# Performance work log

Measured on AMD Instinct MI355X. Metric: run time of the kernel, lower is better.

The kernel has to match this reference:

```python
import jax, jax.numpy as jnp
import numpy as np

ALPHA = 0.2
NEG = -9e15


def _gru(x, Wih, Whh, bih, bhh):
    # x: [B, T, F]; PyTorch nn.GRU cell equations, scan over time.
    H = Whh.shape[1]
    xg = jnp.einsum('btf,gf->btg', x, Wih) + bih  # [B,T,3H]

    def step(h, gi):
        gh = h @ Whh.T + bhh
        ir, iz, inn = jnp.split(gi, 3, axis=-1)
        hr, hz, hn = jnp.split(gh, 3, axis=-1)
        r = jax.nn.sigmoid(ir + hr)
        z = jax.nn.sigmoid(iz + hz)
        n = jnp.tanh(inn + r * hn)
        h = (1.0 - z) * n + z * h
        return h, h

    h0 = jnp.zeros((x.shape[0], H), x.dtype)
    _, ys = jax.lax.scan(step, h0, jnp.swapaxes(xg, 0, 1))
    return jnp.swapaxes(ys, 0, 1)  # [B,T,H]


def _gru_attn(x, Wih, Whh, bih, bhh, aw, ab):
    out = _gru(x, Wih, Whh, bih, bhh)              # [B,T,H]
    w = jax.nn.softmax(out @ aw + ab, axis=1)       # [B,T,1]
    return jnp.sum(out * w, axis=1)                 # [B,H]


def _gat(h, mask, W, a):
    # GraphAttentionLayer with concat=True: elu(softmax(mask(leakyrelu(Wh1+Wh2^T))) @ Wh)
    Wh = h @ W                                      # [N,O]
    O = W.shape[1]
    e = jax.nn.leaky_relu((Wh @ a[:O]) + (Wh @ a[O:]).T, ALPHA)  # [N,N]
    att = jax.nn.softmax(jnp.where(mask, e, NEG), axis=1)
    return jax.nn.elu(att @ Wh)


def setup_inputs() -> dict:
    key = jax.random.key(0)
    ks = iter(jax.random.split(key, 40))
    B, S, Wk, D, F = 1, 2048, 32, 5, 16
    H, E, NS = 128, 128, 16

    def rn(shape, scale=0.1):
        return jax.random.normal(next(ks), shape, jnp.float32) * scale

    inp = {
        'stock_features': jax.random.normal(next(ks), (B, S, Wk, D, F), jnp.float32),
        'stock_to_sector': jax.random.randint(next(ks), (S,), 0, NS, jnp.int32),
        'inter_adj': jax.random.randint(next(ks), (NS, NS), 0, 2, jnp.int32),
        'gru1_Wih': rn((3 * H, F)), 'gru1_Whh': rn((3 * H, H)),
        'gru1_bih': rn((3 * H,)), 'gru1_bhh': rn((3 * H,)),
        'attn1_w': rn((H, 1)), 'attn1_b': rn((1,)),
        'gat_intra_W': rn((H, E)), 'gat_intra_a': rn((2 * E, 1)),
        'grug_Wih': rn((3 * E, E)), 'grug_Whh': rn((3 * E, E)),
        'grug_bih': rn((3 * E,)), 'grug_bhh': rn((3 * E,)),
        'attng_w': rn((E, 1)), 'attng_b': rn((1,)),
        'grua_Wih': rn((3 * E, H)), 'grua_Whh': rn((3 * E, E)),
        'grua_bih': rn((3 * E,)), 'grua_bhh': rn((3 * E,)),
        'attna_w': rn((E, 1)), 'attna_b': rn((1,)),
        'gat_inter_W': rn((E, E)), 'gat_inter_a': rn((2 * E, 1)),
        'fusion_w': rn((3 * E, E)), 'fusion_b': rn((E,)),
        'ret_w': rn((E, 1)), 'ret_b': rn((1,)),
        'mov_w': rn((E, 1)), 'mov_b': rn((1,)),
    }
    return inp


def reference(stock_features, stock_to_sector, inter_adj,
              gru1_Wih, gru1_Whh, gru1_bih, gru1_bhh, attn1_w, attn1_b,
              gat_intra_W, gat_intra_a,
              grug_Wih, grug_Whh, grug_bih, grug_bhh, attng_w, attng_b,
              grua_Wih, grua_Whh, grua_bih, grua_bhh, attna_w, attna_b,
              gat_inter_W, gat_inter_a,
              fusion_w, fusion_b, ret_w, ret_b, mov_w, mov_b):
    B, S, Wk, D, F = stock_features.shape
    H = gru1_Whh.shape[1]
    E = gat_intra_W.shape[1]
    NS = inter_adj.shape[0]

    # Short-term: GRU-attention over days, vectorized over (batch, stock, week).
    x = stock_features.reshape(B * S * Wk, D, F)
    short = _gru_attn(x, gru1_Wih, gru1_Whh, gru1_bih, gru1_bhh, attn1_w, attn1_b)
    short = short.reshape(B, S, Wk, H)

    # Intra-sector GAT on last-week embeddings; per-sector softmax == block mask.
    same_sector = stock_to_sector[:, None] == stock_to_sector[None, :]  # [S,S]
    last = short[:, :, -1, :]                                            # [B,S,H]
    intra = jax.vmap(lambda h: _gat(h, same_sector, gat_intra_W, gat_intra_a))(last)  # [B,S,E]

    # Long-term GRU-attentions.
    lg = _gru_attn(intra.reshape(B * S, 1, E), grug_Wih, grug_Whh, grug_bih, grug_bhh,
                   attng_w, attng_b).reshape(B, S, E)
    la = _gru_attn(short.reshape(B * S, Wk, H), grua_Wih, grua_Whh, grua_bih, grua_bhh,
                   attna_w, attna_b).reshape(B, S, E)

    # Sector embeddings = mean of stock long-term embeddings per sector.
    def sector_mean(g):
        sums = jax.ops.segment_sum(g, stock_to_sector, num_segments=NS)
        cnt = jax.ops.segment_sum(jnp.ones((g.shape[0], 1), g.dtype),
                                  stock_to_sector, num_segments=NS)
        return sums / jnp.maximum(cnt, 1.0)

    sec = jax.vmap(sector_mean)(lg)                                      # [B,NS,E]
    imask = inter_adj > 0
    sec_out = jax.vmap(lambda h: _gat(h, imask, gat_inter_W, gat_inter_a))(sec)
    sec_ps = sec_out[:, stock_to_sector, :]                               # [B,S,E]

    fused = jnp.concatenate([lg, la, sec_ps], axis=-1) @ fusion_w + fusion_b
    returns = (fused @ ret_w + ret_b)[..., 0]
    moves = jax.nn.sigmoid(fused @ mov_w + mov_b)[..., 0]
    return jnp.stack([returns, moves])  # [2,B,S]
```

## Files before the change

kernel.cpp:

```cpp
#include <hip/hip_runtime.h>
#include <math.h>

#define LRELU_A 0.2f
#define NEGBIG (-9.0e15f)

typedef _Float16 f16;
typedef _Float16 f16x8 __attribute__((ext_vector_type(8)));
typedef _Float16 f16x4 __attribute__((ext_vector_type(4)));
typedef _Float16 f16x2 __attribute__((ext_vector_type(2)));
typedef float floatx4 __attribute__((ext_vector_type(4)));

__device__ __forceinline__ float rcpf(float x){ return __builtin_amdgcn_rcpf(x); }
__device__ __forceinline__ float sigm(float x){ return rcpf(1.0f+__expf(-x)); }
__device__ __forceinline__ float gru_fuse(float xr, float xz, float xn_pre, float ghn, float h){
    float Er = __expf(-xr);
    float r  = rcpf(1.0f + Er);
    float En = __expf(2.0f*(xn_pre + r*ghn));
    float Ez = __expf(-xz);
    float Dn = En + 1.0f;
    float num = fmaf(h, Dn, (En - 1.0f)*Ez);
    float den = Dn * (1.0f + Ez);
    return num * rcpf(den);
}
__device__ __forceinline__ f16x8 load_cvt8(const float* __restrict__ p){
    float4 a = *(const float4*)p; float4 b = *(const float4*)(p+4);
    f16x8 r; r[0]=(f16)a.x; r[1]=(f16)a.y; r[2]=(f16)a.z; r[3]=(f16)a.w;
    r[4]=(f16)b.x; r[5]=(f16)b.y; r[6]=(f16)b.z; r[7]=(f16)b.w;
    return r;
}
#define MFMA16(A,B,C) __builtin_amdgcn_mfma_f32_16x16x32_f16((A),(B),(C),0,0,0)

__global__ __launch_bounds__(256) void prep1_kernel(
    const float* __restrict__ g1Wih, const float* __restrict__ g1Whh,
    f16* __restrict__ Wcat1)
{
    const int b = blockIdx.x, tid = threadIdx.x;
    for (int idx = b*256+tid; idx < 512*160; idx += 160*256){
        int r = idx/160, k = idx - r*160;
        float v = 0.0f;
        if (r < 256){ if (k < 32){ if (k < 16) v = g1Wih[r*16+k]; } else v = g1Whh[r*128 + (k-32)]; }
        else if (r < 384){ if (k < 16) v = g1Wih[r*16+k]; }
        else { if (k >= 32) v = g1Whh[(r-128)*128 + (k-32)]; }
        Wcat1[idx] = (f16)v;
    }
}

__global__ __launch_bounds__(512,2) void gru_short(
    const float* __restrict__ x, const f16* __restrict__ Wcat,
    const float* __restrict__ bih, const float* __restrict__ bhh,
    const float* __restrict__ aw, const float* __restrict__ ab,
    f16* __restrict__ out,
    const float* __restrict__ gaWih, const float* __restrict__ gaWhh,
    const float* __restrict__ giW,   const float* __restrict__ fw,
    const float* __restrict__ geW,   const float* __restrict__ ggWih,
    const int* __restrict__ sec,
    f16* __restrict__ WcatA, f16* __restrict__ WTp, f16* __restrict__ fwp,
    f16* __restrict__ gep,   f16* __restrict__ ggp,
    int* __restrict__ memflat, int* __restrict__ pos,
    int* __restrict__ cnt, int* __restrict__ base)
{
    __shared__ __align__(16) f16 xs[5][32][40];
    __shared__ __align__(16) f16 hs[2][32][136];
    __shared__ float scpart[2][8][32];
    __shared__ int cs[16], wsc[16];
    const int tid = threadIdx.x, w = tid>>6, lane = tid&63;
    const int c = lane&15, quad = lane>>4;

    if (blockIdx.x >= 256){
        const int b2 = blockIdx.x - 256;
        if (b2 < 256){
            int idx = b2*512 + tid;
            int r = idx >> 8, k = idx & 255;
            float v = 0.0f;
            if (r < 256){ v = (k < 128) ? gaWih[r*128+k] : gaWhh[r*128 + (k-128)]; }
            else if (r < 384){ if (k < 128) v = gaWih[r*128+k]; }
            else { if (k >= 128) v = gaWhh[(r-128)*128 + (k-128)]; }
            WcatA[idx] = (f16)v;
        } else if (b2 < 288){
            int idx = (b2-256)*512 + tid;
            int e=idx&7, ln=(idx>>3)&63, fr=idx>>9;
            int kb=fr&3, jb=fr>>2;
            int k = kb*32 + (ln>>4)*8 + e, col = jb*16 + (ln&15);
            WTp[idx] = (f16)giW[k*128 + col];
        } else if (b2 < 384){
            int idx = (b2-288)*512 + tid;
            int e=idx&7, ln=(idx>>3)&63, fr=idx>>9;
            int kb=fr%12, jb=fr/12;
            int k = kb*32 + (ln>>4)*8 + e, col = jb*16 + (ln&15);
            fwp[idx] = (f16)fw[k*128 + col];
        } else if (b2 < 416){
            int idx = (b2-384)*512 + tid;
            int e=idx&7, ln=(idx>>3)&63, fr=idx>>9;
            int kb=fr&3, jb=fr>>2;
            int k = kb*32 + (ln>>4)*8 + e, col = jb*16 + (ln&15);
            gep[idx] = (f16)geW[k*128 + col];
        } else if (b2 < 512){
            int idx = (b2-416)*512 + tid;
            int e=idx&7, ln=(idx>>3)&63, fr=idx>>9;
            int kb=fr&3, jb=(fr>>2)&7, G=fr>>5;
            int row = G*128 + jb*16 + (ln&15), k = kb*32 + (ln>>4)*8 + e;
            ggp[idx] = (f16)ggWih[row*128 + k];
        } else {
            if (tid < 16) cs[tid] = 0;
            __syncthreads();
            for (int s = tid; s < 2048; s += 512) atomicAdd(&cs[sec[s]], 1);
            __syncthreads();
            if (tid == 0){
                int acc = 0;
                for (int g=0; g<16; g++){ cnt[g]=cs[g]; base[g]=acc; wsc[g]=acc; acc+=cs[g]; }
            }
            __syncthreads();
            for (int s = tid; s < 2048; s += 512){
                int g = sec[s];
                int p2 = atomicAdd(&wsc[g], 1);
                memflat[p2] = s;
                pos[s] = p2;
            }
        }
        return;
    }
    { f16x4 z4 = {0,0,0,0};
      f16x4* zx = (f16x4*)&xs[0][0][0];
      for (int i=tid; i<1600; i+=512) zx[i] = z4; }

    const int jrow = w*16 + c;
    f16x8 Ar[5], Az[5], Agi, Agh[4];
#pragma unroll
    for (int kb=0;kb<5;kb++){
        Ar[kb] = *(const f16x8*)&Wcat[(size_t)(jrow)*160 + kb*32 + quad*8];
        Az[kb] = *(const f16x8*)&Wcat[(size_t)(128+jrow)*160 + kb*32 + quad*8];
    }
    Agi = *(const f16x8*)&Wcat[(size_t)(256+jrow)*160 + quad*8];
#pragma unroll
    for (int i=0;i<4;i++)
        Agh[i] = *(const f16x8*)&Wcat[(size_t)(384+jrow)*160 + 32 + i*32 + quad*8];

    float brz_r[4], brz_z[4], b_in[4], b_hn[4], awr[4];
#pragma unroll
    for (int r=0;r<4;r++){
        int j = w*16 + quad*4 + r;
        brz_r[r] = bih[j] + bhh[j];
        brz_z[r] = bih[128+j] + bhh[128+j];
        b_in[r] = bih[256+j]; b_hn[r] = bhh[256+j];
        awr[r] = aw[j];
    }
    const float abv = ab[0];

    const int s0i = tid/20,        q0 = tid - 20*s0i;
    const int i1  = tid + 512;
    const int s1i = i1/20,         q1 = i1 - 20*s1i;
    const bool pf1 = (tid < 128);
    float4 xpf0, xpf1;
    {
        const size_t base0 = (size_t)(blockIdx.x*8)*32;
        xpf0 = *(const float4*)&x[(base0 + s0i)*80 + q0*4];
        if (pf1) xpf1 = *(const float4*)&x[(base0 + s1i)*80 + q1*4];
    }

#pragma unroll 1
    for (int tile=0; tile<8; ++tile){
        const int s0 = (blockIdx.x*8 + tile)*32;
        {
            int t = (q0*4)>>4, f = (q0*4)&15;
            f16x4 h4; h4[0]=(f16)xpf0.x; h4[1]=(f16)xpf0.y; h4[2]=(f16)xpf0.z; h4[3]=(f16)xpf0.w;
            *(f16x4*)&xs[t][s0i][f] = h4;
            if (pf1){
                int t1 = (q1*4)>>4, f1 = (q1*4)&15;
                f16x4 g4; g4[0]=(f16)xpf1.x; g4[1]=(f16)xpf1.y; g4[2]=(f16)xpf1.z; g4[3]=(f16)xpf1.w;
                *(f16x4*)&xs[t1][s1i][f1] = g4;
            }
        }
        if (tile < 7){
            const size_t basen = (size_t)(s0 + 32);
            xpf0 = *(const float4*)&x[(basen + s0i)*80 + q0*4];
            if (pf1) xpf1 = *(const float4*)&x[(basen + s1i)*80 + q1*4];
        }
        float hreg[2][4], aacc[2][4], l_[2] = {0.0f, 0.0f};
#pragma unroll
        for (int st=0; st<2; st++)
#pragma unroll
            for (int r=0;r<4;r++){ aacc[st][r]=0.0f; }
        __syncthreads();

        {
            float sp[2];
#pragma unroll
            for (int st=0; st<2; st++){
                f16x8 Bx = *(const f16x8*)&xs[0][st*16+c][quad*8];
                floatx4 ar = {0,0,0,0}, az = {0,0,0,0}, agi = {0,0,0,0};
                ar = MFMA16(Ar[0], Bx, ar);
                az = MFMA16(Az[0], Bx, az);
                agi = MFMA16(Agi, Bx, agi);
                f16x4 h4;
                sp[st] = 0.0f;
#pragma unroll
                for (int r=0;r<4;r++){
                    float hn = gru_fuse(ar[r] + brz_r[r], az[r] + brz_z[r],
                                        agi[r] + b_in[r], b_hn[r], 0.0f);
                    hreg[st][r] = hn; h4[r] = (f16)hn;
                    sp[st] += hn * awr[r];
                }
                *(f16x4*)&hs[0][st*16 + c][w*16 + quad*4] = h4;
            }
#pragma unroll
            for (int st=0; st<2; st++){
                sp[st] += __shfl_xor(sp[st], 16);
                sp[st] += __shfl_xor(sp[st], 32);
            }
            if (lane < 16){ scpart[0][w][lane] = sp[0]; scpart[0][w][16+lane] = sp[1]; }
            __syncthreads();
        }

#pragma unroll 1
        for (int t=1; t<5; ++t){
            const int rp = (t&1)^1, wp = t&1;
            f16x8 Bx[2], Bh[2][4];
#pragma unroll
            for (int st=0; st<2; st++){
                Bx[st] = *(const f16x8*)&xs[t][st*16+c][quad*8];
#pragma unroll
                for (int i=0;i<4;i++)
                    Bh[st][i] = *(const f16x8*)&hs[rp][st*16+c][i*32+quad*8];
            }
            {
#pragma unroll
                for (int st=0; st<2; st++){
                    float sc = abv;
#pragma unroll
                    for (int ww=0; ww<8; ww++) sc += scpart[rp][ww][st*16+c];
                    float e = __expf(sc);
                    l_[st] += e;
#pragma unroll
                    for (int r=0;r<4;r++) aacc[st][r] += e*hreg[st][r];
                }
            }
            float sp[2];
#pragma unroll
            for (int st=0; st<2; st++){
                floatx4 ar = {0,0,0,0}, az = {0,0,0,0}, agi = {0,0,0,0}, agh = {0,0,0,0};
                ar = MFMA16(Ar[0], Bx[st], ar);
                az = MFMA16(Az[0], Bx[st], az);
                agi = MFMA16(Agi, Bx[st], agi);
#pragma unroll
                for (int i=0;i<4;i++){
                    ar = MFMA16(Ar[1+i], Bh[st][i], ar);
                    az = MFMA16(Az[1+i], Bh[st][i], az);
                    agh = MFMA16(Agh[i], Bh[st][i], agh);
                }
                f16x4 h4;
                sp[st] = 0.0f;
#pragma unroll
                for (int r=0;r<4;r++){
                    float hn = gru_fuse(ar[r] + brz_r[r], az[r] + brz_z[r],
                                        agi[r] + b_in[r], agh[r] + b_hn[r], hreg[st][r]);
                    hreg[st][r] = hn; h4[r] = (f16)hn;
                    sp[st] += hn * awr[r];
                }
                *(f16x4*)&hs[wp][st*16 + c][w*16 + quad*4] = h4;
            }
#pragma unroll
            for (int st=0; st<2; st++){
                sp[st] += __shfl_xor(sp[st], 16);
                sp[st] += __shfl_xor(sp[st], 32);
            }
            if (lane < 16){ scpart[wp][w][lane] = sp[0]; scpart[wp][w][16+lane] = sp[1]; }
            __syncthreads();
        }
#pragma unroll
        for (int st=0; st<2; st++){
            float sc = abv;
#pragma unroll
            for (int ww=0; ww<8; ww++) sc += scpart[0][ww][st*16+c];
            float e = __expf(sc);
            l_[st] += e;
            float inv = rcpf(l_[st]);
            f16x4 h4;
#pragma unroll
            for (int r=0;r<4;r++) h4[r] = (f16)((aacc[st][r] + e*hreg[st][r])*inv);
            *(f16x4*)&out[(size_t)(s0 + st*16 + c)*128 + w*16 + quad*4] = h4;
        }
    }
}

__global__ __launch_bounds__(512,2) void gru_la_gatprep(
    const f16* __restrict__ xseq, const f16* __restrict__ Wcat,
    const float* __restrict__ bih, const float* __restrict__ bhh,
    const float* __restrict__ aw, const float* __restrict__ ab,
    f16* __restrict__ out,
    const f16* __restrict__ WTp, const float* __restrict__ gia,
    const int* __restrict__ memflat,
    f16* __restrict__ Whs, float* __restrict__ ers, float* __restrict__ el)
{
    __shared__ __align__(16) f16 xs[2][16][136];
    __shared__ __align__(16) f16 hs[2][16][136];
    __shared__ float scpart[2][8][16];
    __shared__ __align__(16) float tbuf[32][132];
    __shared__ int rows[32];
    const int tid = threadIdx.x, w = tid>>6, lane = tid&63;
    const int c = lane&15, quad = lane>>4;

    if (blockIdx.x >= 256){
        const int p0 = (blockIdx.x-256)*32;
        if (tid < 32) rows[tid] = memflat[p0 + tid];
        __syncthreads();
        f16x8 A[2][4];
#pragma unroll
        for (int mt=0;mt<2;mt++)
#pragma unroll
            for (int kb=0;kb<4;kb++)
                A[mt][kb] = *(const f16x8*)&xseq[((size_t)rows[mt*16+c]*32 + 31)*128 + kb*32 + quad*8];
        {
            f16x8 B[4];
#pragma unroll
            for (int kb=0;kb<4;kb++)
                B[kb] = *(const f16x8*)&WTp[(((size_t)(w*4+kb))*64 + lane)*8];
            floatx4 acc[2] = {{0,0,0,0},{0,0,0,0}};
#pragma unroll
            for (int kb=0;kb<4;kb++){
                acc[0] = MFMA16(A[0][kb], B[kb], acc[0]);
                acc[1] = MFMA16(A[1][kb], B[kb], acc[1]);
            }
#pragma unroll
            for (int mt=0;mt<2;mt++)
#pragma unroll
                for (int r=0;r<4;r++)
                    tbuf[mt*16 + quad*4 + r][w*16 + c] = acc[mt][r];
        }
        __syncthreads();
        for (int i=tid; i<1024; i+=512){
            int s = i>>5, p = i&31;
            float4 v = *(const float4*)&tbuf[s][p*4];
            f16x4 h4; h4[0]=(f16)v.x; h4[1]=(f16)v.y; h4[2]=(f16)v.z; h4[3]=(f16)v.w;
            *(f16x4*)&Whs[(size_t)(p0+s)*128 + p*4] = h4;
        }
        for (int k=0; k<4; k++){
            int row = w*4 + k;
            float w0 = tbuf[row][lane], w1 = tbuf[row][64+lane];
            float v1 = w0*gia[lane]     + w1*gia[64+lane];
            float v2 = w0*gia[128+lane] + w1*gia[192+lane];
#pragma unroll
            for (int off=32; off; off>>=1){ v1 += __shfl_down(v1,off); v2 += __shfl_down(v2,off); }
            if (lane==0){ el[rows[row]] = v1; ers[p0+row] = v2; }
        }
        return;
    }
    const int s0 = blockIdx.x*8;
    if (tid < 128){
        int s = tid>>4, p = tid&15;
        *(f16x8*)&xs[0][s][p*8] = *(const f16x8*)&xseq[((size_t)(s0+s)*32 + 0)*128 + p*8];
    }
    const int jrow = w*16 + c;
    f16x8 Ar[8], Az[8], Agi[4], Agh[4];
#pragma unroll
    for (int kb=0;kb<8;kb++){
        Ar[kb] = *(const f16x8*)&Wcat[(size_t)(jrow)*256 + kb*32 + quad*8];
        Az[kb] = *(const f16x8*)&Wcat[(size_t)(128+jrow)*256 + kb*32 + quad*8];
    }
#pragma unroll
    for (int i=0;i<4;i++){
        Agi[i] = *(const f16x8*)&Wcat[(size_t)(256+jrow)*256 + i*32 + quad*8];
        Agh[i] = *(const f16x8*)&Wcat[(size_t)(384+jrow)*256 + 128 + i*32 + quad*8];
    }
    float brz_r[4], brz_z[4], b_in[4], b_hn[4], awr[4];
#pragma unroll
    for (int r=0;r<4;r++){
        int j = w*16 + quad*4 + r;
        brz_r[r] = bih[j] + bhh[j];
        brz_z[r] = bih[128+j] + bhh[128+j];
        b_in[r] = bih[256+j]; b_hn[r] = bhh[256+j];
        awr[r] = aw[j];
    }
    const float abv = ab[0];
    float hreg[4] = {0,0,0,0}, aacc[4] = {0,0,0,0}, l_ = 0.0f;
    __syncthreads();

    {
        f16x8 Bx[4];
#pragma unroll
        for (int i=0;i<4;i++) Bx[i] = *(const f16x8*)&xs[0][c][i*32+quad*8];
        f16x8 xstage;
        if (tid < 128){
            int s = tid>>4, p = tid&15;
            xstage = *(const f16x8*)&xseq[((size_t)(s0+s)*32 + 1)*128 + p*8];
        }
        floatx4 ar = {0,0,0,0}, az = {0,0,0,0}, agi = {0,0,0,0};
#pragma unroll
        for (int i=0;i<4;i++){
            ar  = MFMA16(Ar[i],  Bx[i], ar);
            az  = MFMA16(Az[i],  Bx[i], az);
            agi = MFMA16(Agi[i], Bx[i], agi);
        }
        f16x4 h4;
        float sp = 0.0f;
#pragma unroll
        for (int r=0;r<4;r++){
            float hn = gru_fuse(ar[r] + brz_r[r], az[r] + brz_z[r],
                                agi[r] + b_in[r], b_hn[r], 0.0f);
            hreg[r] = hn; h4[r] = (f16)hn;
            sp += hn * awr[r];
        }
        *(f16x4*)&hs[0][c][w*16 + quad*4] = h4;
        if (tid < 128){
            int s = tid>>4, p = tid&15;
            *(f16x8*)&xs[1][s][p*8] = xstage;
        }
        sp += __shfl_xor(sp, 16);
        sp += __shfl_xor(sp, 32);
        if (lane < 16) scpart[0][w][lane] = sp;
        __syncthreads();
    }

#pragma unroll 1
    for (int t=1; t<32; ++t){
        const int rp = (t&1)^1, wp = t&1, xp = t&1;
        f16x8 Bx[4], Bh[4];
#pragma unroll
        for (int i=0;i<4;i++){
            Bx[i] = *(const f16x8*)&xs[xp][c][i*32+quad*8];
            Bh[i] = *(const f16x8*)&hs[rp][c][i*32+quad*8];
        }
        f16x8 xstage;
        const bool do_stage = (t < 31) && (tid < 128);
        if (do_stage){
            int s = tid>>4, p = tid&15;
            xstage = *(const f16x8*)&xseq[((size_t)(s0+s)*32 + t+1)*128 + p*8];
        }
        {
            float sc = abv;
#pragma unroll
            for (int ww=0; ww<8; ww++) sc += scpart[rp][ww][c];
            float e = __expf(sc);
            l_ += e;
#pragma unroll
            for (int r=0;r<4;r++) aacc[r] += e*hreg[r];
        }
        floatx4 ar = {0,0,0,0}, az = {0,0,0,0}, agi = {0,0,0,0}, agh = {0,0,0,0};
#pragma unroll
        for (int i=0;i<4;i++){
            ar = MFMA16(Ar[i], Bx[i], ar);
            az = MFMA16(Az[i], Bx[i], az);
            agi = MFMA16(Agi[i], Bx[i], agi);
        }
#pragma unroll
        for (int i=0;i<4;i++){
            ar = MFMA16(Ar[4+i], Bh[i], ar);
            az = MFMA16(Az[4+i], Bh[i], az);
            agh = MFMA16(Agh[i], Bh[i], agh);
        }
        f16x4 h4;
        float sp = 0.0f;
#pragma unroll
        for (int r=0;r<4;r++){
            float hn = gru_fuse(ar[r] + brz_r[r], az[r] + brz_z[r],
                                agi[r] + b_in[r], agh[r] + b_hn[r], hreg[r]);
            hreg[r] = hn; h4[r] = (f16)hn;
            sp += hn * awr[r];
        }
        *(f16x4*)&hs[wp][c][w*16 + quad*4] = h4;
        if (do_stage){
            int s = tid>>4, p = tid&15;
            *(f16x8*)&xs[xp^1][s][p*8] = xstage;
        }
        sp += __shfl_xor(sp, 16);
        sp += __shfl_xor(sp, 32);
        if (lane < 16) scpart[wp][w][lane] = sp;
        __syncthreads();
    }
    {
        float sc = abv;
#pragma unroll
        for (int ww=0; ww<8; ww++) sc += scpart[1][ww][c];
        float e = __expf(sc);
        l_ += e;
        float inv = rcpf(l_);
        f16x4 h4;
#pragma unroll
        for (int r=0;r<4;r++) h4[r] = (f16)((aacc[r] + e*hreg[r])*inv);
        if (c < 8)
            *(f16x4*)&out[(size_t)(s0 + c)*128 + w*16 + quad*4] = h4;
    }
}

__global__ __launch_bounds__(256) void gat_intra_mem_kernel(
    const f16* __restrict__ Whs, const float* __restrict__ ers,
    const float* __restrict__ el, const int* __restrict__ sec,
    const int* __restrict__ cnt, const int* __restrict__ base,
    f16* __restrict__ outp, int S)
{
    int wave = threadIdx.x>>6, lane = threadIdx.x&63;
    int i = blockIdx.x*4 + wave;
    if (i>=S) return;
    int g = sec[i];
    int n = cnt[g], b = base[g];
    float eli = el[i];
    float m = -INFINITY;
    for (int jj=lane; jj<n; jj+=64){
        float v = eli + ers[b+jj]; v = v>0.f? v : LRELU_A*v;
        m = fmaxf(m, v);
    }
#pragma unroll
    for (int off=32; off; off>>=1) m = fmaxf(m, __shfl_xor(m, off));
    float l = 0.f, c0=0.f, c1=0.f;
#pragma unroll 8
    for (int jj=0; jj<n; jj++){
        float v = eli + ers[b+jj]; v = v>0.f? v : LRELU_A*v;
        float p = __expf(v-m);
        l += p;
        f16x2 wv = *(const f16x2*)&Whs[(size_t)(b+jj)*128 + lane*2];
        c0 += p*(float)wv[0];
        c1 += p*(float)wv[1];
    }
    float il = rcpf(l);
    c0 *= il; c1 *= il;
    f16x2 o;
    o[0] = (f16)(c0>0.f? c0 : expm1f(c0));
    o[1] = (f16)(c1>0.f? c1 : expm1f(c1));
    *(f16x2*)&outp[(size_t)i*128 + lane*2] = o;
}

__global__ __launch_bounds__(256) void lg_mfma(
    const f16* __restrict__ intra16, const f16* __restrict__ ggp,
    const float* __restrict__ bih, const float* __restrict__ bhh,
    const int* __restrict__ pos,
    f16* __restrict__ lgout, f16* __restrict__ lgs)
{
    __shared__ __align__(16) f16 tbuf[16][136];
    const int tid = threadIdx.x, w = tid>>6, lane = tid&63;
    const int c = lane&15, quad = lane>>4;
    const int s0 = blockIdx.x*16;
    f16x8 A[4];
#pragma unroll
    for (int kb=0;kb<4;kb++)
        A[kb] = *(const f16x8*)&intra16[(size_t)(s0+c)*128 + kb*32 + quad*8];
#pragma unroll
    for (int i=0;i<2;i++){
        int jb = w*2 + i;
        int j = jb*16 + c;
        f16x8 Br[4], Bz[4], Bn[4];
#pragma unroll
        for (int kb=0;kb<4;kb++){
            Br[kb] = *(const f16x8*)&ggp[(((size_t)((0*8+jb)*4+kb))*64 + lane)*8];
            Bz[kb] = *(const f16x8*)&ggp[(((size_t)((1*8+jb)*4+kb))*64 + lane)*8];
            Bn[kb] = *(const f16x8*)&ggp[(((size_t)((2*8+jb)*4+kb))*64 + lane)*8];
        }
        float b_r = bih[j] + bhh[j];
        float b_z = bih[128+j] + bhh[128+j];
        float b_i = bih[256+j], b_h = bhh[256+j];
        floatx4 ar = {0,0,0,0}, az = {0,0,0,0}, an = {0,0,0,0};
#pragma unroll
        for (int kb=0;kb<4;kb++){
            ar = MFMA16(A[kb], Br[kb], ar);
            az = MFMA16(A[kb], Bz[kb], az);
            an = MFMA16(A[kb], Bn[kb], an);
        }
#pragma unroll
        for (int r=0;r<4;r++){
            float Er = __expf(-(ar[r] + b_r));
            float rg = rcpf(1.0f + Er);
            float En = __expf(2.0f*(an[r] + b_i + rg*b_h));
            float Ez = __expf(-(az[r] + b_z));
            float v = (En - 1.0f)*Ez * rcpf((En + 1.0f)*(1.0f + Ez));
            tbuf[quad*4 + r][j] = (f16)v;
        }
    }
    __syncthreads();
    {
        int s = tid>>4, p = tid&15;
        f16x8 v = *(const f16x8*)&tbuf[s][p*8];
        *(f16x8*)&lgout[(size_t)(s0+s)*128 + p*8] = v;
        *(f16x8*)&lgs[(size_t)pos[s0+s]*128 + p*8] = v;
    }
}

__global__ __launch_bounds__(1024) void gat_inter_fused(
    const f16* __restrict__ lgs, const int* __restrict__ cnt,
    const int* __restrict__ base, const int* __restrict__ adj,
    const f16* __restrict__ gep, const float* __restrict__ a,
    float* __restrict__ outp)
{
    __shared__ __align__(16) float hs[16][132];
    __shared__ __align__(16) float Whs[16][132];
    __shared__ float el[16], er[16];
    __shared__ float att[16][16];
    const int tid = threadIdx.x, w = tid>>6, lane = tid&63;
    const int c = lane&15, quad = lane>>4;

    {
        int n = cnt[w], b = base[w];
        const int rowoff = lane>>4;
        const int colb = (lane&15)*8;
        float acc[8] = {0,0,0,0,0,0,0,0};
        for (int r = rowoff; r < n; r += 4){
            f16x8 v = *(const f16x8*)&lgs[(size_t)(b+r)*128 + colb];
#pragma unroll
            for (int k=0;k<8;k++) acc[k] += (float)v[k];
        }
#pragma unroll
        for (int k=0;k<8;k++){
            acc[k] += __shfl_xor(acc[k], 16);
            acc[k] += __shfl_xor(acc[k], 32);
        }
        if (lane < 16){
            float inv = rcpf(fmaxf((float)n, 1.0f));
#pragma unroll
            for (int k=0;k<8;k++) hs[w][colb+k] = acc[k]*inv;
        }
    }
    __syncthreads();
    if (w < 8){
        f16x8 A[4], B[4];
#pragma unroll
        for (int kb=0;kb<4;kb++){
            A[kb] = load_cvt8(&hs[c][kb*32 + quad*8]);
            B[kb] = *(const f16x8*)&gep[(((size_t)(w*4+kb))*64 + lane)*8];
        }
        floatx4 acc = {0,0,0,0};
#pragma unroll
        for (int kb=0;kb<4;kb++) acc = MFMA16(A[kb], B[kb], acc);
#pragma unroll
        for (int r=0;r<4;r++) Whs[quad*4 + r][w*16 + c] = acc[r];
    }
    __syncthreads();
    {
        int half = lane>>5, l = lane&31;
        const float* av = a + half*128;
        float acc2 = 0.f;
#pragma unroll
        for (int k=0;k<4;k++) acc2 += Whs[w][l+32*k]*av[l+32*k];
#pragma unroll
        for (int off=1; off<32; off<<=1) acc2 += __shfl_xor(acc2, off);
        if (l==0){ if (half) er[w]=acc2; else el[w]=acc2; }
    }
    __syncthreads();
    if (tid<16){
        int i=tid; float m=NEGBIG; float e[16];
        for(int j=0;j<16;j++){
            float v = el[i]+er[j]; v = v>0.f? v : LRELU_A*v;
            e[j] = (adj[i*16+j]>0)? v : NEGBIG;
            m = fmaxf(m,e[j]);
        }
        float l=0.f;
        for(int j=0;j<16;j++){ float p=__expf(e[j]-m); att[i][j]=p; l+=p; }
        float il = rcpf(l);
        for(int j=0;j<16;j++) att[i][j] *= il;
    }
    __syncthreads();
#pragma unroll
    for (int i=0;i<2;i++){
        int idx=i*1024+tid; int o=idx&127, s=idx>>7;
        float acc=0.f;
#pragma unroll
        for(int j=0;j<16;j++) acc += att[s][j]*Whs[j][o];
        outp[s*128+o] = acc>0.f? acc : expm1f(acc);
    }
}

__global__ __launch_bounds__(256) void fused_mfma(
    const f16* __restrict__ lg16, const f16* __restrict__ la16,
    const float* __restrict__ seco, const int* __restrict__ sec,
    const f16* __restrict__ fwp,
    const float* __restrict__ fb, const float* __restrict__ rw,
    const float* __restrict__ rb, const float* __restrict__ mw,
    const float* __restrict__ mb, float* __restrict__ outp)
{
    __shared__ float rpart[4][16], mpart[4][16];
    const int tid = threadIdx.x, w = tid>>6, lane = tid&63;
    const int c = lane&15, quad = lane>>4;
    const int s0 = blockIdx.x*16;
    f16x8 A[12];
    {
        int row = s0 + c;
        int g = sec[row];
#pragma unroll
        for (int kb=0;kb<4;kb++){
            A[kb]   = *(const f16x8*)&lg16[(size_t)row*128 + kb*32 + quad*8];
            A[4+kb] = *(const f16x8*)&la16[(size_t)row*128 + kb*32 + quad*8];
            A[8+kb] = load_cvt8(&seco[(size_t)g*128 + kb*32 + quad*8]);
        }
    }
    float rsum[4] = {0,0,0,0};
    float msum[4] = {0,0,0,0};
#pragma unroll
    for (int i=0;i<2;i++){
        int jb = w*2 + i;
        int col = jb*16 + c;
        f16x8 B[12];
#pragma unroll
        for (int kb=0;kb<12;kb++)
            B[kb] = *(const f16x8*)&fwp[(((size_t)(jb*12+kb))*64 + lane)*8];
        floatx4 acc = {0,0,0,0};
#pragma unroll
        for (int kb=0;kb<12;kb++)
            acc = MFMA16(A[kb], B[kb], acc);
        float fbv = fb[col], rwv = rw[col], mwv = mw[col];
#pragma unroll
        for (int r=0;r<4;r++){
            float fu = acc[r] + fbv;
            rsum[r] += fu*rwv;
            msum[r] += fu*mwv;
        }
    }
#pragma unroll
    for (int r=0;r<4;r++){
#pragma unroll
        for (int off=1; off<16; off<<=1){
            rsum[r] += __shfl_xor(rsum[r], off);
            msum[r] += __shfl_xor(msum[r], off);
        }
        if (c==0){
            rpart[w][quad*4 + r] = rsum[r];
            mpart[w][quad*4 + r] = msum[r];
        }
    }
    __syncthreads();
    if (tid < 16){
        int s = tid;
        float rs = rb[0], ms = mb[0];
#pragma unroll
        for (int ww=0; ww<4; ww++){ rs += rpart[ww][s]; ms += mpart[ww][s]; }
        outp[s0+s] = rs;
        outp[2048 + s0 + s] = sigm(ms);
    }
}

extern "C" void kernel_launch(void* const* d_in, const int* in_sizes, int n_in,
                              void* d_out, int out_size, void* d_ws, size_t ws_size,
                              hipStream_t stream) {
    const float* sf    = (const float*)d_in[0];
    const int*   sec   = (const int*)  d_in[1];
    const int*   adj   = (const int*)  d_in[2];
    const float* g1Wih = (const float*)d_in[3];
    const float* g1Whh = (const float*)d_in[4];
    const float* g1bih = (const float*)d_in[5];
    const float* g1bhh = (const float*)d_in[6];
    const float* a1w   = (const float*)d_in[7];
    const float* a1b   = (const float*)d_in[8];
    const float* giW   = (const float*)d_in[9];
    const float* gia   = (const float*)d_in[10];
    const float* ggWih = (const float*)d_in[11];
    const float* ggbih = (const float*)d_in[13];
    const float* ggbhh = (const float*)d_in[14];
    const float* gaWih = (const float*)d_in[17];
    const float* gaWhh = (const float*)d_in[18];
    const float* gabih = (const float*)d_in[19];
    const float* gabhh = (const float*)d_in[20];
    const float* aaw   = (const float*)d_in[21];
    const float* aab   = (const float*)d_in[22];
    const float* geW   = (const float*)d_in[23];
    const float* gea   = (const float*)d_in[24];
    const float* fw    = (const float*)d_in[25];
    const float* fb    = (const float*)d_in[26];
    const float* rw    = (const float*)d_in[27];
    const float* rb    = (const float*)d_in[28];
    const float* mw    = (const float*)d_in[29];
    const float* mb    = (const float*)d_in[30];

    char* p = (char*)d_ws;
    f16*   shrt16 = (f16*)p;   p += (size_t)65536*128*2;
    f16*   intra16= (f16*)p;   p += (size_t)262144*2;
    f16*   lg16   = (f16*)p;   p += (size_t)262144*2;
    f16*   la16   = (f16*)p;   p += (size_t)262144*2;
    f16*   Whs    = (f16*)p;   p += (size_t)262144*2;
    f16*   lgs    = (f16*)p;   p += (size_t)262144*2;
    f16*   Wcat1  = (f16*)p;   p += (size_t)512*160*2;
    f16*   WcatA  = (f16*)p;   p += (size_t)512*256*2;
    f16*   WTp    = (f16*)p;   p += (size_t)16384*2;
    f16*   gep    = (f16*)p;   p += (size_t)16384*2;
    f16*   fwp    = (f16*)p;   p += (size_t)49152*2;
    f16*   ggp    = (f16*)p;   p += (size_t)49152*2;
    float* el     = (float*)p; p += 2048*4;
    float* ers    = (float*)p; p += 2048*4;
    float* seco   = (float*)p; p += 2048*4;
    int*   memflat= (int*)p;   p += 2048*4;
    int*   pos    = (int*)p;   p += 2048*4;
    int*   cnt    = (int*)p;   p += 16*4;
    int*   basep  = (int*)p;   p += 16*4;

    prep1_kernel<<<160,256,0,stream>>>(g1Wih, g1Whh, Wcat1);
    gru_short<<<769,512,0,stream>>>(sf, Wcat1, g1bih, g1bhh, a1w, a1b, shrt16,
                                    gaWih, gaWhh, giW, fw, geW, ggWih, sec,
                                    WcatA, WTp, fwp, gep, ggp,
                                    memflat, pos, cnt, basep);
    gru_la_gatprep<<<320,512,0,stream>>>(shrt16, WcatA, gabih, gabhh, aaw, aab, la16,
                                         WTp, gia, memflat, Whs, ers, el);
    gat_intra_mem_kernel<<<512,256,0,stream>>>(Whs, ers, el, sec, cnt, basep, intra16, 2048);
    lg_mfma<<<128,256,0,stream>>>(intra16, ggp, ggbih, ggbhh, pos, lg16, lgs);
    gat_inter_fused<<<1,1024,0,stream>>>(lgs, cnt, basep, adj, gep, gea, seco);
    fused_mfma<<<128,256,0,stream>>>(lg16, la16, seco, sec, fwp, fb, rw, rb, mw, mb, (float*)d_out);
}
```

Measured before the change: 275.8 us.

## Fuse tail kernels into one launch chained by global atomic flags

Merges the four tail kernels (intra GAT, long-term GRU step, inter-sector GAT and fusion head) into a single 513-block launch. Block ranges take each stage and hand off through global atomic counters with acquire spin-waits, replacing kernel-boundary sync and three launch gaps. Flags are reset in the prep kernel. This relies on earlier blocks being scheduled before the waiting ones, which holds for the grid size but risks deadlock if dispatch order changes, and the waiting blocks hold CU slots while they spin.

```diff
diff --git a/kernel.cpp b/kernel.cpp
--- a/kernel.cpp
+++ b/kernel.cpp
@@ -30,11 +30,17 @@
 }
 #define MFMA16(A,B,C) __builtin_amdgcn_mfma_f32_16x16x32_f16((A),(B),(C),0,0,0)
 
+__device__ __forceinline__ void wait_flag(int* f, int target){
+    while (__hip_atomic_load(f, __ATOMIC_ACQUIRE, __HIP_MEMORY_SCOPE_AGENT) < target)
+        __builtin_amdgcn_s_sleep(32);
+}
+
 __global__ __launch_bounds__(256) void prep1_kernel(
     const float* __restrict__ g1Wih, const float* __restrict__ g1Whh,
-    f16* __restrict__ Wcat1)
+    f16* __restrict__ Wcat1, int* __restrict__ flags)
 {
     const int b = blockIdx.x, tid = threadIdx.x;
+    if (b == 0 && tid < 4) flags[tid] = 0;
     for (int idx = b*256+tid; idx < 512*160; idx += 160*256){
         int r = idx/160, k = idx - r*160;
         float v = 0.0f;
@@ -481,245 +487,258 @@
     }
 }
 
-__global__ __launch_bounds__(256) void gat_intra_mem_kernel(
+__global__ __launch_bounds__(512,2) void tail_chain(
     const f16* __restrict__ Whs, const float* __restrict__ ers,
     const float* __restrict__ el, const int* __restrict__ sec,
     const int* __restrict__ cnt, const int* __restrict__ base,
-    f16* __restrict__ outp, int S)
-{
-    int wave = threadIdx.x>>6, lane = threadIdx.x&63;
-    int i = blockIdx.x*4 + wave;
-    if (i>=S) return;
-    int g = sec[i];
-    int n = cnt[g], b = base[g];
-    float eli = el[i];
-    float m = -INFINITY;
-    for (int jj=lane; jj<n; jj+=64){
-        float v = eli + ers[b+jj]; v = v>0.f? v : LRELU_A*v;
-        m = fmaxf(m, v);
-    }
-#pragma unroll
-    for (int off=32; off; off>>=1) m = fmaxf(m, __shfl_xor(m, off));
-    float l = 0.f, c0=0.f, c1=0.f;
-#pragma unroll 8
-    for (int jj=0; jj<n; jj++){
-        float v = eli + ers[b+jj]; v = v>0.f? v : LRELU_A*v;
-        float p = __expf(v-m);
-        l += p;
-        f16x2 wv = *(const f16x2*)&Whs[(size_t)(b+jj)*128 + lane*2];
-        c0 += p*(float)wv[0];
-        c1 += p*(float)wv[1];
-    }
-    float il = rcpf(l);
-    c0 *= il; c1 *= il;
-    f16x2 o;
-    o[0] = (f16)(c0>0.f? c0 : expm1f(c0));
-    o[1] = (f16)(c1>0.f? c1 : expm1f(c1));
-    *(f16x2*)&outp[(size_t)i*128 + lane*2] = o;
-}
-
-__global__ __launch_bounds__(256) void lg_mfma(
-    const f16* __restrict__ intra16, const f16* __restrict__ ggp,
-    const float* __restrict__ bih, const float* __restrict__ bhh,
-    const int* __restrict__ pos,
-    f16* __restrict__ lgout, f16* __restrict__ lgs)
-{
-    __shared__ __align__(16) f16 tbuf[16][136];
-    const int tid = threadIdx.x, w = tid>>6, lane = tid&63;
-    const int c = lane&15, quad = lane>>4;
-    const int s0 = blockIdx.x*16;
-    f16x8 A[4];
-#pragma unroll
-    for (int kb=0;kb<4;kb++)
-        A[kb] = *(const f16x8*)&intra16[(size_t)(s0+c)*128 + kb*32 + quad*8];
-#pragma unroll
-    for (int i=0;i<2;i++){
-        int jb = w*2 + i;
-        int j = jb*16 + c;
-        f16x8 Br[4], Bz[4], Bn[4];
-#pragma unroll
-        for (int kb=0;kb<4;kb++){
-            Br[kb] = *(const f16x8*)&ggp[(((size_t)((0*8+jb)*4+kb))*64 + lane)*8];
-            Bz[kb] = *(const f16x8*)&ggp[(((size_t)((1*8+jb)*4+kb))*64 + lane)*8];
-            Bn[kb] = *(const f16x8*)&ggp[(((size_t)((2*8+jb)*4+kb))*64 + lane)*8];
-        }
-        float b_r = bih[j] + bhh[j];
-        float b_z = bih[128+j] + bhh[128+j];
-        float b_i = bih[256+j], b_h = bhh[256+j];
-        floatx4 ar = {0,0,0,0}, az = {0,0,0,0}, an = {0,0,0,0};
-#pragma unroll
-        for (int kb=0;kb<4;kb++){
-            ar = MFMA16(A[kb], Br[kb], ar);
-            az = MFMA16(A[kb], Bz[kb], az);
-            an = MFMA16(A[kb], Bn[kb], an);
-        }
-#pragma unroll
-        for (int r=0;r<4;r++){
-            float Er = __expf(-(ar[r] + b_r));
-            float rg = rcpf(1.0f + Er);
-            float En = __expf(2.0f*(an[r] + b_i + rg*b_h));
-            float Ez = __expf(-(az[r] + b_z));
-            float v = (En - 1.0f)*Ez * rcpf((En + 1.0f)*(1.0f + Ez));
-            tbuf[quad*4 + r][j] = (f16)v;
-        }
-    }
-    __syncthreads();
-    {
-        int s = tid>>4, p = tid&15;
-        f16x8 v = *(const f16x8*)&tbuf[s][p*8];
-        *(f16x8*)&lgout[(size_t)(s0+s)*128 + p*8] = v;
-        *(f16x8*)&lgs[(size_t)pos[s0+s]*128 + p*8] = v;
-    }
-}
-
-__global__ __launch_bounds__(1024) void gat_inter_fused(
-    const f16* __restrict__ lgs, const int* __restrict__ cnt,
-    const int* __restrict__ base, const int* __restrict__ adj,
-    const f16* __restrict__ gep, const float* __restrict__ a,
-    float* __restrict__ outp)
-{
-    __shared__ __align__(16) float hs[16][132];
-    __shared__ __align__(16) float Whs[16][132];
-    __shared__ float el[16], er[16];
-    __shared__ float att[16][16];
-    const int tid = threadIdx.x, w = tid>>6, lane = tid&63;
-    const int c = lane&15, quad = lane>>4;
-
-    {
-        int n = cnt[w], b = base[w];
-        const int rowoff = lane>>4;
-        const int colb = (lane&15)*8;
-        float acc[8] = {0,0,0,0,0,0,0,0};
-        for (int r = rowoff; r < n; r += 4){
-            f16x8 v = *(const f16x8*)&lgs[(size_t)(b+r)*128 + colb];
-#pragma unroll
-            for (int k=0;k<8;k++) acc[k] += (float)v[k];
-        }
-#pragma unroll
-        for (int k=0;k<8;k++){
-            acc[k] += __shfl_xor(acc[k], 16);
-            acc[k] += __shfl_xor(acc[k], 32);
-        }
-        if (lane < 16){
-            float inv = rcpf(fmaxf((float)n, 1.0f));
-#pragma unroll
-            for (int k=0;k<8;k++) hs[w][colb+k] = acc[k]*inv;
-        }
-    }
-    __syncthreads();
-    if (w < 8){
-        f16x8 A[4], B[4];
-#pragma unroll
-        for (int kb=0;kb<4;kb++){
-            A[kb] = load_cvt8(&hs[c][kb*32 + quad*8]);
-            B[kb] = *(const f16x8*)&gep[(((size_t)(w*4+kb))*64 + lane)*8];
-        }
-        floatx4 acc = {0,0,0,0};
-#pragma unroll
-        for (int kb=0;kb<4;kb++) acc = MFMA16(A[kb], B[kb], acc);
-#pragma unroll
-        for (int r=0;r<4;r++) Whs[quad*4 + r][w*16 + c] = acc[r];
-    }
-    __syncthreads();
-    {
-        int half = lane>>5, l = lane&31;
-        const float* av = a + half*128;
-        float acc2 = 0.f;
-#pragma unroll
-        for (int k=0;k<4;k++) acc2 += Whs[w][l+32*k]*av[l+32*k];
-#pragma unroll
-        for (int off=1; off<32; off<<=1) acc2 += __shfl_xor(acc2, off);
-        if (l==0){ if (half) er[w]=acc2; else el[w]=acc2; }
-    }
-    __syncthreads();
-    if (tid<16){
-        int i=tid; float m=NEGBIG; float e[16];
-        for(int j=0;j<16;j++){
-            float v = el[i]+er[j]; v = v>0.f? v : LRELU_A*v;
-            e[j] = (adj[i*16+j]>0)? v : NEGBIG;
-            m = fmaxf(m,e[j]);
-        }
-        float l=0.f;
-        for(int j=0;j<16;j++){ float p=__expf(e[j]-m); att[i][j]=p; l+=p; }
-        float il = rcpf(l);
-        for(int j=0;j<16;j++) att[i][j] *= il;
-    }
-    __syncthreads();
-#pragma unroll
-    for (int i=0;i<2;i++){
-        int idx=i*1024+tid; int o=idx&127, s=idx>>7;
-        float acc=0.f;
-#pragma unroll
-        for(int j=0;j<16;j++) acc += att[s][j]*Whs[j][o];
-        outp[s*128+o] = acc>0.f? acc : expm1f(acc);
-    }
-}
-
-__global__ __launch_bounds__(256) void fused_mfma(
-    const f16* __restrict__ lg16, const f16* __restrict__ la16,
-    const float* __restrict__ seco, const int* __restrict__ sec,
-    const f16* __restrict__ fwp,
+    f16* __restrict__ intra16,
+    const f16* __restrict__ ggp, const float* __restrict__ ggbih,
+    const float* __restrict__ ggbhh, const int* __restrict__ pos,
+    f16* __restrict__ lg16, f16* __restrict__ lgs,
+    const int* __restrict__ adj, const f16* __restrict__ gep,
+    const float* __restrict__ gea, float* __restrict__ seco,
+    const f16* __restrict__ la16, const f16* __restrict__ fwp,
     const float* __restrict__ fb, const float* __restrict__ rw,
     const float* __restrict__ rb, const float* __restrict__ mw,
-    const float* __restrict__ mb, float* __restrict__ outp)
+    const float* __restrict__ mb, float* __restrict__ outp,
+    int* __restrict__ flags)
 {
+    __shared__ __align__(16) f16 tbuf16[16][136];
+    __shared__ __align__(16) float ths[16][132];
+    __shared__ __align__(16) float tWhs[16][132];
+    __shared__ float tel[16], ter[16], tatt[16][16];
     __shared__ float rpart[4][16], mpart[4][16];
     const int tid = threadIdx.x, w = tid>>6, lane = tid&63;
     const int c = lane&15, quad = lane>>4;
-    const int s0 = blockIdx.x*16;
-    f16x8 A[12];
+    const int b = blockIdx.x;
+
+    if (b < 256){
+        int i = b*8 + w;
+        int g = sec[i];
+        int n = cnt[g], bb = base[g];
+        float eli = el[i];
+        float m = -INFINITY;
+        for (int jj=lane; jj<n; jj+=64){
+            float v = eli + ers[bb+jj]; v = v>0.f? v : LRELU_A*v;
+            m = fmaxf(m, v);
+        }
+#pragma unroll
+        for (int off=32; off; off>>=1) m = fmaxf(m, __shfl_xor(m, off));
+        float l = 0.f, c0=0.f, c1=0.f;
+#pragma unroll 8
+        for (int jj=0; jj<n; jj++){
+            float v = eli + ers[bb+jj]; v = v>0.f? v : LRELU_A*v;
+            float p = __expf(v-m);
+            l += p;
+            f16x2 wv = *(const f16x2*)&Whs[(size_t)(bb+jj)*128 + lane*2];
+            c0 += p*(float)wv[0];
+            c1 += p*(float)wv[1];
+        }
+        float il = rcpf(l);
+        c0 *= il; c1 *= il;
+        f16x2 o;
+        o[0] = (f16)(c0>0.f? c0 : expm1f(c0));
+        o[1] = (f16)(c1>0.f? c1 : expm1f(c1));
+        *(f16x2*)&intra16[(size_t)i*128 + lane*2] = o;
+        __threadfence();
+        __syncthreads();
+        if (tid == 0) atomicAdd(&flags[0], 1);
+        return;
+    }
+    if (b < 384){
+        if (tid == 0) wait_flag(&flags[0], 256);
+        __syncthreads();
+        __threadfence();
+        const int s0 = (b-256)*16;
+        if (tid < 256){
+            f16x8 A[4];
+#pragma unroll
+            for (int kb=0;kb<4;kb++)
+                A[kb] = *(const f16x8*)&intra16[(size_t)(s0+c)*128 + kb*32 + quad*8];
+#pragma unroll
+            for (int i=0;i<2;i++){
+                int jb = w*2 + i;
+                int j = jb*16 + c;
+                f16x8 Br[4], Bz[4], Bn[4];
+#pragma unroll
+                for (int kb=0;kb<4;kb++){
+                    Br[kb] = *(const f16x8*)&ggp[(((size_t)((0*8+jb)*4+kb))*64 + lane)*8];
+                    Bz[kb] = *(const f16x8*)&ggp[(((size_t)((1*8+jb)*4+kb))*64 + lane)*8];
+                    Bn[kb] = *(const f16x8*)&ggp[(((size_t)((2*8+jb)*4+kb))*64 + lane)*8];
+                }
+                float b_r = ggbih[j] + ggbhh[j];
+                float b_z = ggbih[128+j] + ggbhh[128+j];
+                float b_i = ggbih[256+j], b_h = ggbhh[256+j];
+                floatx4 ar = {0,0,0,0}, az = {0,0,0,0}, an = {0,0,0,0};
+#pragma unroll
+                for (int kb=0;kb<4;kb++){
+                    ar = MFMA16(A[kb], Br[kb], ar);
+                    az = MFMA16(A[kb], Bz[kb], az);
+                    an = MFMA16(A[kb], Bn[kb], an);
+                }
+#pragma unroll
+                for (int r=0;r<4;r++){
+                    float Er = __expf(-(ar[r] + b_r));
+                    float rg = rcpf(1.0f + Er);
+                    float En = __expf(2.0f*(an[r] + b_i + rg*b_h));
+                    float Ez = __expf(-(az[r] + b_z));
+                    float v = (En - 1.0f)*Ez * rcpf((En + 1.0f)*(1.0f + Ez));
+                    tbuf16[quad*4 + r][j] = (f16)v;
+                }
+            }
+        }
+        __syncthreads();
+        if (tid < 256){
+            int s = tid>>4, p = tid&15;
+            f16x8 v = *(const f16x8*)&tbuf16[s][p*8];
+            *(f16x8*)&lg16[(size_t)(s0+s)*128 + p*8] = v;
+            *(f16x8*)&lgs[(size_t)pos[s0+s]*128 + p*8] = v;
+        }
+        __threadfence();
+        __syncthreads();
+        if (tid == 0) atomicAdd(&flags[1], 1);
+        return;
+    }
+    if (b == 384){
+        if (tid == 0) wait_flag(&flags[1], 128);
+        __syncthreads();
+        __threadfence();
+#pragma unroll 1
+        for (int g = w; g < 16; g += 8){
+            int n = cnt[g], bb = base[g];
+            const int rowoff = lane>>4;
+            const int colb = (lane&15)*8;
+            float acc[8] = {0,0,0,0,0,0,0,0};
+            for (int r = rowoff; r < n; r += 4){
+                f16x8 v = *(const f16x8*)&lgs[(size_t)(bb+r)*128 + colb];
+#pragma unroll
+                for (int k=0;k<8;k++) acc[k] += (float)v[k];
+            }
+#pragma unroll
+            for (int k=0;k<8;k++){
+                acc[k] += __shfl_xor(acc[k], 16);
+                acc[k] += __shfl_xor(acc[k], 32);
+            }
+            if (lane < 16){
+                float inv = rcpf(fmaxf((float)n, 1.0f));
+#pragma unroll
+                for (int k=0;k<8;k++) ths[g][colb+k] = acc[k]*inv;
+            }
+        }
+        __syncthreads();
+        {
+            f16x8 A[4], B[4];
+#pragma unroll
+            for (int kb=0;kb<4;kb++){
+                A[kb] = load_cvt8(&ths[c][kb*32 + quad*8]);
+                B[kb] = *(const f16x8*)&gep[(((size_t)(w*4+kb))*64 + lane)*8];
+            }
+            floatx4 acc = {0,0,0,0};
+#pragma unroll
+            for (int kb=0;kb<4;kb++) acc = MFMA16(A[kb], B[kb], acc);
+#pragma unroll
+            for (int r=0;r<4;r++) tWhs[quad*4 + r][w*16 + c] = acc[r];
+        }
+        __syncthreads();
+#pragma unroll 1
+        for (int g = w; g < 16; g += 8){
+            int half = lane>>5, l = lane&31;
+            const float* av = gea + half*128;
+            float acc2 = 0.f;
+#pragma unroll
+            for (int k=0;k<4;k++) acc2 += tWhs[g][l+32*k]*av[l+32*k];
+#pragma unroll
+            for (int off=1; off<32; off<<=1) acc2 += __shfl_xor(acc2, off);
+            if (l==0){ if (half) ter[g]=acc2; else tel[g]=acc2; }
+        }
+        __syncthreads();
+        if (tid<16){
+            int i=tid; float m=NEGBIG; float e[16];
+            for(int j=0;j<16;j++){
+                float v = tel[i]+ter[j]; v = v>0.f? v : LRELU_A*v;
+                e[j] = (adj[i*16+j]>0)? v : NEGBIG;
+                m = fmaxf(m,e[j]);
+            }
+            float l=0.f;
+            for(int j=0;j<16;j++){ float p=__expf(e[j]-m); tatt[i][j]=p; l+=p; }
+            float il = rcpf(l);
+            for(int j=0;j<16;j++) tatt[i][j] *= il;
+        }
+        __syncthreads();
+#pragma unroll
+        for (int i=0;i<4;i++){
+            int idx=i*512+tid; int o=idx&127, s=idx>>7;
+            float acc=0.f;
+#pragma unroll
+            for(int j=0;j<16;j++) acc += tatt[s][j]*tWhs[j][o];
+            seco[s*128+o] = acc>0.f? acc : expm1f(acc);
+        }
+        __threadfence();
+        __syncthreads();
+        if (tid == 0) atomicAdd(&flags[2], 1);
+        return;
+    }
     {
-        int row = s0 + c;
-        int g = sec[row];
-#pragma unroll
-        for (int kb=0;kb<4;kb++){
-            A[kb]   = *(const f16x8*)&lg16[(size_t)row*128 + kb*32 + quad*8];
-            A[4+kb] = *(const f16x8*)&la16[(size_t)row*128 + kb*32 + quad*8];
-            A[8+kb] = load_cvt8(&seco[(size_t)g*128 + kb*32 + quad*8]);
-        }
-    }
-    float rsum[4] = {0,0,0,0};
-    float msum[4] = {0,0,0,0};
-#pragma unroll
-    for (int i=0;i<2;i++){
-        int jb = w*2 + i;
-        int col = jb*16 + c;
-        f16x8 B[12];
-#pragma unroll
-        for (int kb=0;kb<12;kb++)
-            B[kb] = *(const f16x8*)&fwp[(((size_t)(jb*12+kb))*64 + lane)*8];
-        floatx4 acc = {0,0,0,0};
-#pragma unroll
-        for (int kb=0;kb<12;kb++)
-            acc = MFMA16(A[kb], B[kb], acc);
-        float fbv = fb[col], rwv = rw[col], mwv = mw[col];
-#pragma unroll
-        for (int r=0;r<4;r++){
-            float fu = acc[r] + fbv;
-            rsum[r] += fu*rwv;
-            msum[r] += fu*mwv;
-        }
-    }
-#pragma unroll
-    for (int r=0;r<4;r++){
-#pragma unroll
-        for (int off=1; off<16; off<<=1){
-            rsum[r] += __shfl_xor(rsum[r], off);
-            msum[r] += __shfl_xor(msum[r], off);
-        }
-        if (c==0){
-            rpart[w][quad*4 + r] = rsum[r];
-            mpart[w][quad*4 + r] = msum[r];
-        }
-    }
-    __syncthreads();
-    if (tid < 16){
-        int s = tid;
-        float rs = rb[0], ms = mb[0];
-#pragma unroll
-        for (int ww=0; ww<4; ww++){ rs += rpart[ww][s]; ms += mpart[ww][s]; }
-        outp[s0+s] = rs;
-        outp[2048 + s0 + s] = sigm(ms);
+        if (tid == 0) wait_flag(&flags[2], 1);
+        __syncthreads();
+        __threadfence();
+        const int s0 = (b-385)*16;
+        float rsum[4] = {0,0,0,0};
+        float msum[4] = {0,0,0,0};
+        if (tid < 256){
+            f16x8 A[12];
+            {
+                int row = s0 + c;
+                int g = sec[row];
+#pragma unroll
+                for (int kb=0;kb<4;kb++){
+                    A[kb]   = *(const f16x8*)&lg16[(size_t)row*128 + kb*32 + quad*8];
+                    A[4+kb] = *(const f16x8*)&la16[(size_t)row*128 + kb*32 + quad*8];
+                    A[8+kb] = load_cvt8(&seco[(size_t)g*128 + kb*32 + quad*8]);
+                }
+            }
+#pragma unroll
+            for (int i=0;i<2;i++){
+                int jb = w*2 + i;
+                int col = jb*16 + c;
+                f16x8 B[12];
+#pragma unroll
+                for (int kb=0;kb<12;kb++)
+                    B[kb] = *(const f16x8*)&fwp[(((size_t)(jb*12+kb))*64 + lane)*8];
+                floatx4 acc = {0,0,0,0};
+#pragma unroll
+                for (int kb=0;kb<12;kb++)
+                    acc = MFMA16(A[kb], B[kb], acc);
+                float fbv = fb[col], rwv = rw[col], mwv = mw[col];
+#pragma unroll
+                for (int r=0;r<4;r++){
+                    float fu = acc[r] + fbv;
+                    rsum[r] += fu*rwv;
+                    msum[r] += fu*mwv;
+                }
+            }
+#pragma unroll
+            for (int r=0;r<4;r++){
+#pragma unroll
+                for (int off=1; off<16; off<<=1){
+                    rsum[r] += __shfl_xor(rsum[r], off);
+                    msum[r] += __shfl_xor(msum[r], off);
+                }
+                if (c==0){
+                    rpart[w][quad*4 + r] = rsum[r];
+                    mpart[w][quad*4 + r] = msum[r];
+                }
+            }
+        }
+        __syncthreads();
+        if (tid < 16){
+            int s = tid;
+            float rs = rb[0], ms = mb[0];
+#pragma unroll
+            for (int ww=0; ww<4; ww++){ rs += rpart[ww][s]; ms += mpart[ww][s]; }
+            outp[s0+s] = rs;
+            outp[2048 + s0 + s] = sigm(ms);
+        }
     }
 }
 
@@ -775,16 +794,18 @@
     int*   pos    = (int*)p;   p += 2048*4;
     int*   cnt    = (int*)p;   p += 16*4;
     int*   basep  = (int*)p;   p += 16*4;
-
-    prep1_kernel<<<160,256,0,stream>>>(g1Wih, g1Whh, Wcat1);
+    int*   flags  = (int*)p;   p += 4*4;
+
+    prep1_kernel<<<160,256,0,stream>>>(g1Wih, g1Whh, Wcat1, flags);
     gru_short<<<769,512,0,stream>>>(sf, Wcat1, g1bih, g1bhh, a1w, a1b, shrt16,
                                     gaWih, gaWhh, giW, fw, geW, ggWih, sec,
                                     WcatA, WTp, fwp, gep, ggp,
                                     memflat, pos, cnt, basep);
     gru_la_gatprep<<<320,512,0,stream>>>(shrt16, WcatA, gabih, gabhh, aaw, aab, la16,
                                          WTp, gia, memflat, Whs, ers, el);
-    gat_intra_mem_kernel<<<512,256,0,stream>>>(Whs, ers, el, sec, cnt, basep, intra16, 2048);
-    lg_mfma<<<128,256,0,stream>>>(intra16, ggp, ggbih, ggbhh, pos, lg16, lgs);
-    gat_inter_fused<<<1,1024,0,stream>>>(lgs, cnt, basep, adj, gep, gea, seco);
-    fused_mfma<<<128,256,0,stream>>>(lg16, la16, seco, sec, fwp, fb, rw, rb, mw, mb, (float*)d_out);
+    tail_chain<<<513,512,0,stream>>>(Whs, ers, el, sec, cnt, basep, intra16,
+                                     ggp, ggbih, ggbhh, pos, lg16, lgs,
+                                     adj, gep, gea, seco,
+                                     la16, fwp, fb, rw, rb, mw, mb,
+                                     (float*)d_out, flags);
 }
```

Result: slower. 506.3 us (+83.6%).
